# Optimization experiments

Hardware: AMD Instinct MI355X
Metric: run time of the kernel (lower is better)

The kernel has to match this reference:

```python
import jax, jax.numpy as jnp
import numpy as np

BS, N, D = 4, 512, 128

def setup_inputs() -> dict:
    key = jax.random.key(0)
    ks = jax.random.split(key, 8)
    s = 1.0 / np.sqrt(D)
    return {
        "x":  jax.random.normal(ks[0], (BS, N, D), dtype=jnp.float32),
        "Wq": jax.random.normal(ks[1], (D, D), dtype=jnp.float32) * s,
        "bq": jax.random.normal(ks[2], (D,), dtype=jnp.float32) * s,
        "Wk": jax.random.normal(ks[3], (D, D), dtype=jnp.float32) * s,
        "bk": jax.random.normal(ks[4], (D,), dtype=jnp.float32) * s,
        "Wv": jax.random.normal(ks[5], (D, D), dtype=jnp.float32) * s,
        "bv": jax.random.normal(ks[6], (D,), dtype=jnp.float32) * s,
        "pos_bias": jax.random.normal(ks[7], (N, N), dtype=jnp.float32) * 0.1,
    }

def reference(x, Wq, bq, Wk, bk, Wv, bv, pos_bias):
    # Linear projections (torch Linear: x @ W^T + b)
    q = jax.nn.sigmoid(jnp.einsum('bnd,ed->bne', x, Wq) + bq)   # [B,N,D]
    k = jnp.einsum('bnd,ed->bne', x, Wk) + bk                   # [B,N,D]
    v = jnp.einsum('bnd,ed->bne', x, Wv) + bv                   # [B,N,D]
    # scores[b,t,j,d] = k[b,j,d] + pos_bias[t,j]  (O(n^2 d) intermediate)
    s = k[:, None, :, :] + pos_bias[None, :, :, None]           # [B,N,N,D]
    m = jnp.max(s, axis=2, keepdims=True)                       # stabilizer
    e = jnp.exp(s - m)                                          # [B,N,N,D]
    num = jnp.einsum('btjd,bjd->btd', e, v)                     # [B,N,D]
    den = jnp.sum(e, axis=2)                                    # [B,N,D]
    return q * (num / den)
```

## Files before the change

kernel.cpp:

```cpp
#include <hip/hip_runtime.h>

#define BATCH 4
#define SEQ   512
#define DIM   128

typedef _Float16 half8 __attribute__((ext_vector_type(8)));
typedef _Float16 half4 __attribute__((ext_vector_type(4)));
typedef float    f32x4 __attribute__((ext_vector_type(4)));

__global__ __launch_bounds__(256) void k_prep(
    const float* __restrict__ x, const float* __restrict__ pos,
    const float* __restrict__ Wq, const float* __restrict__ Wk,
    const float* __restrict__ Wv,
    _Float16* __restrict__ x_h, _Float16* __restrict__ ep_h,
    _Float16* __restrict__ wq_h, _Float16* __restrict__ wk_h,
    _Float16* __restrict__ wv_h)
{
    const int blk = blockIdx.x;
    const int tid = threadIdx.x;
    if (blk < 128) {
        const int i = (blk * 256 + tid) * 8;
        const float4 p0 = *(const float4*)(x + i);
        const float4 p1 = *(const float4*)(x + i + 4);
        half8 h;
        h[0]=(_Float16)p0.x; h[1]=(_Float16)p0.y; h[2]=(_Float16)p0.z; h[3]=(_Float16)p0.w;
        h[4]=(_Float16)p1.x; h[5]=(_Float16)p1.y; h[6]=(_Float16)p1.z; h[7]=(_Float16)p1.w;
        *(half8*)(x_h + i) = h;
    } else if (blk < 256) {
        const int i = ((blk - 128) * 256 + tid) * 8;
        const float4 p0 = *(const float4*)(pos + i);
        const float4 p1 = *(const float4*)(pos + i + 4);
        half8 h;
        h[0]=(_Float16)__expf(p0.x); h[1]=(_Float16)__expf(p0.y);
        h[2]=(_Float16)__expf(p0.z); h[3]=(_Float16)__expf(p0.w);
        h[4]=(_Float16)__expf(p1.x); h[5]=(_Float16)__expf(p1.y);
        h[6]=(_Float16)__expf(p1.z); h[7]=(_Float16)__expf(p1.w);
        *(half8*)(ep_h + i) = h;
    } else {
        const int r = blk - 256;
        const float* src = (r < 8) ? Wq : ((r < 16) ? Wk : Wv);
        _Float16* dst    = (r < 8) ? wq_h : ((r < 16) ? wk_h : wv_h);
        const int i = ((r & 7) * 256 + tid) * 8;
        const float4 p0 = *(const float4*)(src + i);
        const float4 p1 = *(const float4*)(src + i + 4);
        half8 h;
        h[0]=(_Float16)p0.x; h[1]=(_Float16)p0.y; h[2]=(_Float16)p0.z; h[3]=(_Float16)p0.w;
        h[4]=(_Float16)p1.x; h[5]=(_Float16)p1.y; h[6]=(_Float16)p1.z; h[7]=(_Float16)p1.w;
        *(half8*)(dst + i) = h;
    }
}

__global__ __launch_bounds__(256) void k_proj(
    const _Float16* __restrict__ x_h,
    const _Float16* __restrict__ wq_h, const float* __restrict__ bq,
    const _Float16* __restrict__ wk_h, const float* __restrict__ bk,
    const _Float16* __restrict__ wv_h, const float* __restrict__ bv,
    float* __restrict__ qout, _Float16* __restrict__ ekk)
{
    const int tid  = threadIdx.x;
    const int lane = tid & 63;
    const int wave = tid >> 6;
    const int l15  = lane & 15;
    const int quad = lane >> 4;

    const int n0 = (blockIdx.x & 7) * 16;
    const int m0 = (blockIdx.x >> 3) * 64 + wave * 16;

    const _Float16* xa = x_h  + (m0 + l15) * DIM + quad * 8;
    const _Float16* wq = wq_h + (n0 + l15) * DIM + quad * 8;
    const _Float16* wk = wk_h + (n0 + l15) * DIM + quad * 8;
    const _Float16* wv = wv_h + (n0 + l15) * DIM + quad * 8;

    f32x4 aq = {0.f, 0.f, 0.f, 0.f};
    f32x4 ak = {0.f, 0.f, 0.f, 0.f};
    f32x4 av = {0.f, 0.f, 0.f, 0.f};

#pragma unroll
    for (int ks = 0; ks < 4; ++ks) {
        const half8 a  = *(const half8*)(xa + ks * 32);
        const half8 b0 = *(const half8*)(wq + ks * 32);
        const half8 b1 = *(const half8*)(wk + ks * 32);
        const half8 b2 = *(const half8*)(wv + ks * 32);
        aq = __builtin_amdgcn_mfma_f32_16x16x32_f16(a, b0, aq, 0, 0, 0);
        ak = __builtin_amdgcn_mfma_f32_16x16x32_f16(a, b1, ak, 0, 0, 0);
        av = __builtin_amdgcn_mfma_f32_16x16x32_f16(a, b2, av, 0, 0, 0);
    }

    const int c   = n0 + l15;
    const float bqv = bq[c];
    const float bkv = bk[c];
    const float bvv = bv[c];

    const int mrow = m0 + quad * 4;
    const int b    = mrow >> 9;
    const int tok  = mrow & 511;

    half4 eh, evh;
#pragma unroll
    for (int r = 0; r < 4; ++r) {
        const float e  = __expf(ak[r] + bkv);
        const float vv = av[r] + bvv;
        const float qv = 1.f / (1.f + __expf(-(aq[r] + bqv)));
        eh[r]  = (_Float16)e;
        evh[r] = (_Float16)(e * vv);
        qout[(b * SEQ + tok + r) * DIM + c] = qv;
    }
    *(half4*)(ekk + ((b * 256) + 2 * c + 0) * SEQ + tok) = eh;
    *(half4*)(ekk + ((b * 256) + 2 * c + 1) * SEQ + tok) = evh;
}

__global__ __launch_bounds__(256) void k_aft(
    const _Float16* __restrict__ ekk,
    const _Float16* __restrict__ ep_h,
    const float* __restrict__ qout,
    float* __restrict__ out)
{
    const int tid  = threadIdx.x;
    const int lane = tid & 63;
    const int wave = tid >> 6;
    const int l15  = lane & 15;
    const int quad = lane >> 4;
    const int wm   = wave & 1;
    const int wn   = wave >> 1;

    const int b  = blockIdx.x >> 6;
    const int m0 = (((blockIdx.x >> 3) & 7) * 32) + wm * 16;
    const int t0 = ((blockIdx.x & 7) * 64) + wn * 32;

    const _Float16* arow  = ekk  + ((b * 256) + m0 + l15) * SEQ + quad * 8;
    const _Float16* brow0 = ep_h + (t0 + l15) * SEQ + quad * 8;
    const _Float16* brow1 = brow0 + 16 * SEQ;

    f32x4 acc0 = {0.f, 0.f, 0.f, 0.f};
    f32x4 acc1 = {0.f, 0.f, 0.f, 0.f};

#pragma unroll
    for (int ks = 0; ks < 16; ++ks) {
        const half8 a  = *(const half8*)(arow  + ks * 32);
        const half8 b0 = *(const half8*)(brow0 + ks * 32);
        const half8 b1 = *(const half8*)(brow1 + ks * 32);
        acc0 = __builtin_amdgcn_mfma_f32_16x16x32_f16(a, b0, acc0, 0, 0, 0);
        acc1 = __builtin_amdgcn_mfma_f32_16x16x32_f16(a, b1, acc1, 0, 0, 0);
    }

    const int d0 = (m0 + quad * 4) >> 1;
#pragma unroll
    for (int i = 0; i < 2; ++i) {
        const f32x4 acc = i ? acc1 : acc0;
        const int t = t0 + i * 16 + l15;
        const float2 qv = *(const float2*)(qout + ((b * SEQ) + t) * DIM + d0);
        float2 o;
        o.x = qv.x * acc[1] / acc[0];
        o.y = qv.y * acc[3] / acc[2];
        *(float2*)(out + ((b * SEQ) + t) * DIM + d0) = o;
    }
}

extern "C" void kernel_launch(void* const* d_in, const int* in_sizes, int n_in,
                              void* d_out, int out_size, void* d_ws, size_t ws_size,
                              hipStream_t stream) {
    const float* x   = (const float*)d_in[0];
    const float* Wq  = (const float*)d_in[1];
    const float* bq  = (const float*)d_in[2];
    const float* Wk  = (const float*)d_in[3];
    const float* bk  = (const float*)d_in[4];
    const float* Wv  = (const float*)d_in[5];
    const float* bv  = (const float*)d_in[6];
    const float* pos = (const float*)d_in[7];

    float* outp = (float*)d_out;
    char*  ws   = (char*)d_ws;

    _Float16* x_h  = (_Float16*)(ws);
    _Float16* ep_h = (_Float16*)(ws + (512 << 10));
    _Float16* ekk  = (_Float16*)(ws + (1024 << 10));
    _Float16* wq_h = (_Float16*)(ws + (2048 << 10));
    _Float16* wk_h = (_Float16*)(ws + (2080 << 10));
    _Float16* wv_h = (_Float16*)(ws + (2112 << 10));
    float*    qout = (float*)   (ws + (2144 << 10));

    k_prep<<<280, 256, 0, stream>>>(x, pos, Wq, Wk, Wv, x_h, ep_h, wq_h, wk_h, wv_h);
    k_proj<<<256, 256, 0, stream>>>(x_h, wq_h, bq, wk_h, bk, wv_h, bv, qout, ekk);
    k_aft<<<256, 256, 0, stream>>>(ekk, ep_h, qout, outp);
}
```

Before: 80.06 us.

## Fuse fp16 conversion into projection kernel and halve AFT tile per block

Removes the separate conversion kernel: the projection kernel now loads fp32 x and weights directly and converts them to fp16 in registers, while extra blocks in the same launch compute exp(pos_bias). This drops one launch and the round trip of the converted x and weights through global memory. The AFT kernel now gives each wave a single 16x16 output tile, doubling the grid to 512 blocks for better occupancy. The cost is redundant fp32 weight loads and conversions in every projection block, and twice the loads of the ekk rows in the AFT stage.

```diff
diff --git a/kernel.cpp b/kernel.cpp
--- a/kernel.cpp
+++ b/kernel.cpp
@@ -8,68 +8,52 @@
 typedef _Float16 half4 __attribute__((ext_vector_type(4)));
 typedef float    f32x4 __attribute__((ext_vector_type(4)));
 
-__global__ __launch_bounds__(256) void k_prep(
-    const float* __restrict__ x, const float* __restrict__ pos,
-    const float* __restrict__ Wq, const float* __restrict__ Wk,
-    const float* __restrict__ Wv,
-    _Float16* __restrict__ x_h, _Float16* __restrict__ ep_h,
-    _Float16* __restrict__ wq_h, _Float16* __restrict__ wk_h,
-    _Float16* __restrict__ wv_h)
+__device__ __forceinline__ half8 ld8h(const float* __restrict__ p) {
+    const float4 a = *(const float4*)p;
+    const float4 b = *(const float4*)(p + 4);
+    half8 h;
+    h[0] = (_Float16)a.x; h[1] = (_Float16)a.y; h[2] = (_Float16)a.z; h[3] = (_Float16)a.w;
+    h[4] = (_Float16)b.x; h[5] = (_Float16)b.y; h[6] = (_Float16)b.z; h[7] = (_Float16)b.w;
+    return h;
+}
+
+__global__ __launch_bounds__(256) void KA(
+    const float* __restrict__ x,
+    const float* __restrict__ Wq, const float* __restrict__ bq,
+    const float* __restrict__ Wk, const float* __restrict__ bk,
+    const float* __restrict__ Wv, const float* __restrict__ bv,
+    const float* __restrict__ pos,
+    float* __restrict__ qout, _Float16* __restrict__ ekk,
+    _Float16* __restrict__ ep_h)
 {
-    const int blk = blockIdx.x;
     const int tid = threadIdx.x;
-    if (blk < 128) {
-        const int i = (blk * 256 + tid) * 8;
-        const float4 p0 = *(const float4*)(x + i);
-        const float4 p1 = *(const float4*)(x + i + 4);
-        half8 h;
-        h[0]=(_Float16)p0.x; h[1]=(_Float16)p0.y; h[2]=(_Float16)p0.z; h[3]=(_Float16)p0.w;
-        h[4]=(_Float16)p1.x; h[5]=(_Float16)p1.y; h[6]=(_Float16)p1.z; h[7]=(_Float16)p1.w;
-        *(half8*)(x_h + i) = h;
-    } else if (blk < 256) {
-        const int i = ((blk - 128) * 256 + tid) * 8;
+    const int bi  = blockIdx.x;
+
+    if (bi >= 256) {
+        const int i = ((bi - 256) * 256 + tid) * 8;
         const float4 p0 = *(const float4*)(pos + i);
         const float4 p1 = *(const float4*)(pos + i + 4);
         half8 h;
-        h[0]=(_Float16)__expf(p0.x); h[1]=(_Float16)__expf(p0.y);
-        h[2]=(_Float16)__expf(p0.z); h[3]=(_Float16)__expf(p0.w);
-        h[4]=(_Float16)__expf(p1.x); h[5]=(_Float16)__expf(p1.y);
-        h[6]=(_Float16)__expf(p1.z); h[7]=(_Float16)__expf(p1.w);
+        h[0] = (_Float16)__expf(p0.x); h[1] = (_Float16)__expf(p0.y);
+        h[2] = (_Float16)__expf(p0.z); h[3] = (_Float16)__expf(p0.w);
+        h[4] = (_Float16)__expf(p1.x); h[5] = (_Float16)__expf(p1.y);
+        h[6] = (_Float16)__expf(p1.z); h[7] = (_Float16)__expf(p1.w);
         *(half8*)(ep_h + i) = h;
-    } else {
-        const int r = blk - 256;
-        const float* src = (r < 8) ? Wq : ((r < 16) ? Wk : Wv);
-        _Float16* dst    = (r < 8) ? wq_h : ((r < 16) ? wk_h : wv_h);
-        const int i = ((r & 7) * 256 + tid) * 8;
-        const float4 p0 = *(const float4*)(src + i);
-        const float4 p1 = *(const float4*)(src + i + 4);
-        half8 h;
-        h[0]=(_Float16)p0.x; h[1]=(_Float16)p0.y; h[2]=(_Float16)p0.z; h[3]=(_Float16)p0.w;
-        h[4]=(_Float16)p1.x; h[5]=(_Float16)p1.y; h[6]=(_Float16)p1.z; h[7]=(_Float16)p1.w;
-        *(half8*)(dst + i) = h;
+        return;
     }
-}
 
-__global__ __launch_bounds__(256) void k_proj(
-    const _Float16* __restrict__ x_h,
-    const _Float16* __restrict__ wq_h, const float* __restrict__ bq,
-    const _Float16* __restrict__ wk_h, const float* __restrict__ bk,
-    const _Float16* __restrict__ wv_h, const float* __restrict__ bv,
-    float* __restrict__ qout, _Float16* __restrict__ ekk)
-{
-    const int tid  = threadIdx.x;
     const int lane = tid & 63;
     const int wave = tid >> 6;
     const int l15  = lane & 15;
     const int quad = lane >> 4;
 
-    const int n0 = (blockIdx.x & 7) * 16;
-    const int m0 = (blockIdx.x >> 3) * 64 + wave * 16;
+    const int n0 = (bi & 7) * 16;
+    const int m0 = (bi >> 3) * 64 + wave * 16;
 
-    const _Float16* xa = x_h  + (m0 + l15) * DIM + quad * 8;
-    const _Float16* wq = wq_h + (n0 + l15) * DIM + quad * 8;
-    const _Float16* wk = wk_h + (n0 + l15) * DIM + quad * 8;
-    const _Float16* wv = wv_h + (n0 + l15) * DIM + quad * 8;
+    const float* xa = x  + (m0 + l15) * DIM + quad * 8;
+    const float* wq = Wq + (n0 + l15) * DIM + quad * 8;
+    const float* wk = Wk + (n0 + l15) * DIM + quad * 8;
+    const float* wv = Wv + (n0 + l15) * DIM + quad * 8;
 
     f32x4 aq = {0.f, 0.f, 0.f, 0.f};
     f32x4 ak = {0.f, 0.f, 0.f, 0.f};
@@ -77,16 +61,16 @@
 
 #pragma unroll
     for (int ks = 0; ks < 4; ++ks) {
-        const half8 a  = *(const half8*)(xa + ks * 32);
-        const half8 b0 = *(const half8*)(wq + ks * 32);
-        const half8 b1 = *(const half8*)(wk + ks * 32);
-        const half8 b2 = *(const half8*)(wv + ks * 32);
+        const half8 a  = ld8h(xa + ks * 32);
+        const half8 b0 = ld8h(wq + ks * 32);
+        const half8 b1 = ld8h(wk + ks * 32);
+        const half8 b2 = ld8h(wv + ks * 32);
         aq = __builtin_amdgcn_mfma_f32_16x16x32_f16(a, b0, aq, 0, 0, 0);
         ak = __builtin_amdgcn_mfma_f32_16x16x32_f16(a, b1, ak, 0, 0, 0);
         av = __builtin_amdgcn_mfma_f32_16x16x32_f16(a, b2, av, 0, 0, 0);
     }
 
-    const int c   = n0 + l15;
+    const int c = n0 + l15;
     const float bqv = bq[c];
     const float bkv = bk[c];
     const float bvv = bv[c];
@@ -109,7 +93,7 @@
     *(half4*)(ekk + ((b * 256) + 2 * c + 1) * SEQ + tok) = evh;
 }
 
-__global__ __launch_bounds__(256) void k_aft(
+__global__ __launch_bounds__(256) void KB(
     const _Float16* __restrict__ ekk,
     const _Float16* __restrict__ ep_h,
     const float* __restrict__ qout,
@@ -120,40 +104,34 @@
     const int wave = tid >> 6;
     const int l15  = lane & 15;
     const int quad = lane >> 4;
-    const int wm   = wave & 1;
-    const int wn   = wave >> 1;
 
-    const int b  = blockIdx.x >> 6;
-    const int m0 = (((blockIdx.x >> 3) & 7) * 32) + wm * 16;
-    const int t0 = ((blockIdx.x & 7) * 64) + wn * 32;
+    const int bi = blockIdx.x;
+    const int b  = bi >> 7;
+    const int mt = (bi >> 4) & 7;
+    const int tt = bi & 15;
 
-    const _Float16* arow  = ekk  + ((b * 256) + m0 + l15) * SEQ + quad * 8;
-    const _Float16* brow0 = ep_h + (t0 + l15) * SEQ + quad * 8;
-    const _Float16* brow1 = brow0 + 16 * SEQ;
+    const int m0 = mt * 32 + (wave & 1) * 16;
+    const int t0 = tt * 32 + (wave >> 1) * 16;
 
-    f32x4 acc0 = {0.f, 0.f, 0.f, 0.f};
-    f32x4 acc1 = {0.f, 0.f, 0.f, 0.f};
+    const _Float16* arow = ekk  + ((b * 256) + m0 + l15) * SEQ + quad * 8;
+    const _Float16* brow = ep_h + (t0 + l15) * SEQ + quad * 8;
+
+    f32x4 acc = {0.f, 0.f, 0.f, 0.f};
 
 #pragma unroll
     for (int ks = 0; ks < 16; ++ks) {
-        const half8 a  = *(const half8*)(arow  + ks * 32);
-        const half8 b0 = *(const half8*)(brow0 + ks * 32);
-        const half8 b1 = *(const half8*)(brow1 + ks * 32);
-        acc0 = __builtin_amdgcn_mfma_f32_16x16x32_f16(a, b0, acc0, 0, 0, 0);
-        acc1 = __builtin_amdgcn_mfma_f32_16x16x32_f16(a, b1, acc1, 0, 0, 0);
+        const half8 a  = *(const half8*)(arow + ks * 32);
+        const half8 b8 = *(const half8*)(brow + ks * 32);
+        acc = __builtin_amdgcn_mfma_f32_16x16x32_f16(a, b8, acc, 0, 0, 0);
     }
 
     const int d0 = (m0 + quad * 4) >> 1;
-#pragma unroll
-    for (int i = 0; i < 2; ++i) {
-        const f32x4 acc = i ? acc1 : acc0;
-        const int t = t0 + i * 16 + l15;
-        const float2 qv = *(const float2*)(qout + ((b * SEQ) + t) * DIM + d0);
-        float2 o;
-        o.x = qv.x * acc[1] / acc[0];
-        o.y = qv.y * acc[3] / acc[2];
-        *(float2*)(out + ((b * SEQ) + t) * DIM + d0) = o;
-    }
+    const int t  = t0 + l15;
+    const float2 qv = *(const float2*)(qout + ((b * SEQ) + t) * DIM + d0);
+    float2 o;
+    o.x = qv.x * acc[1] / acc[0];
+    o.y = qv.y * acc[3] / acc[2];
+    *(float2*)(out + ((b * SEQ) + t) * DIM + d0) = o;
 }
 
 extern "C" void kernel_launch(void* const* d_in, const int* in_sizes, int n_in,
@@ -171,15 +149,10 @@
     float* outp = (float*)d_out;
     char*  ws   = (char*)d_ws;
 
-    _Float16* x_h  = (_Float16*)(ws);
-    _Float16* ep_h = (_Float16*)(ws + (512 << 10));
-    _Float16* ekk  = (_Float16*)(ws + (1024 << 10));
-    _Float16* wq_h = (_Float16*)(ws + (2048 << 10));
-    _Float16* wk_h = (_Float16*)(ws + (2080 << 10));
-    _Float16* wv_h = (_Float16*)(ws + (2112 << 10));
-    float*    qout = (float*)   (ws + (2144 << 10));
+    _Float16* ekk  = (_Float16*)(ws);
+    _Float16* ep_h = (_Float16*)(ws + (1024 << 10));
+    float*    qout = (float*)   (ws + (1536 << 10));
 
-    k_prep<<<280, 256, 0, stream>>>(x, pos, Wq, Wk, Wv, x_h, ep_h, wq_h, wk_h, wv_h);
-    k_proj<<<256, 256, 0, stream>>>(x_h, wq_h, bq, wk_h, bk, wv_h, bv, qout, ekk);
-    k_aft<<<256, 256, 0, stream>>>(ekk, ep_h, qout, outp);
+    KA<<<384, 256, 0, stream>>>(x, Wq, bq, Wk, bk, Wv, bv, pos, qout, ekk, ep_h);
+    KB<<<512, 256, 0, stream>>>(ekk, ep_h, qout, outp);
 }
```

Result: no change. 81.16 us (+1.4%).
